# Performance work log

Hardware: AMD Instinct MI355X
Metric: run time of the kernel (lower is better)

Reference implementation:

```python
import jax, jax.numpy as jnp
import numpy as np

V = 327696       # total nodes (4 graphs x 2 hemis x 40962 verts)
E = 1966080      # directed edges
C = 64           # feature dim
G = 4            # num graphs (subjects)
EPS = 1e-5


def setup_inputs() -> dict:
    key = jax.random.key(0)
    ks = jax.random.split(key, 10)
    x = jax.random.normal(ks[0], (V, C), dtype=jnp.float32)
    edge_index = jax.random.randint(ks[1], (2, E), 0, V, dtype=jnp.int64)
    batch = jnp.sort(jax.random.randint(ks[2], (V,), 0, G, dtype=jnp.int64))
    s = 1.0 / np.sqrt(C)
    return {
        "x": x,
        "edge_index": edge_index,
        "batch": batch,
        # GraphNorm 1 (PyG init: weight=1, bias=0, mean_scale=1)
        "norm1_w": jnp.ones((C,), jnp.float32),
        "norm1_b": jnp.zeros((C,), jnp.float32),
        "norm1_ms": jnp.ones((C,), jnp.float32),
        # SAGEConv linear layers: lin_l (on max-aggregated neighbors, with bias), lin_r (root, no bias)
        "lin_l_w": jax.random.uniform(ks[3], (C, C), jnp.float32, -s, s),
        "lin_l_b": jax.random.uniform(ks[4], (C,), jnp.float32, -s, s),
        "lin_r_w": jax.random.uniform(ks[5], (C, C), jnp.float32, -s, s),
        # GraphNorm 2
        "norm2_w": jnp.ones((C,), jnp.float32),
        "norm2_b": jnp.zeros((C,), jnp.float32),
        "norm2_ms": jnp.ones((C,), jnp.float32),
    }


def graph_norm(x, batch, weight, bias, mean_scale):
    # per-graph mean/var over nodes (PyG GraphNorm)
    ones = jnp.ones((x.shape[0], 1), x.dtype)
    cnt = jax.ops.segment_sum(ones, batch, num_segments=G)            # [G,1]
    mean = jax.ops.segment_sum(x, batch, num_segments=G) / cnt       # [G,C]
    centered = x - mean[batch] * mean_scale
    var = jax.ops.segment_sum(centered * centered, batch, num_segments=G) / cnt
    inv_std = jax.lax.rsqrt(var + EPS)
    return weight * centered * inv_std[batch] + bias


def sage_conv_max(x, edge_index, lin_l_w, lin_l_b, lin_r_w):
    src, dst = edge_index[0], edge_index[1]
    # scatter-max of source features onto destinations (irregular access)
    agg = jax.ops.segment_max(x[src], dst, num_segments=V)
    agg = jnp.where(jnp.isneginf(agg), 0.0, agg)  # nodes with no in-edges -> 0
    return agg @ lin_l_w + lin_l_b + x @ lin_r_w


def reference(x, edge_index, batch, norm1_w, norm1_b, norm1_ms,
              lin_l_w, lin_l_b, lin_r_w, norm2_w, norm2_b, norm2_ms):
    h = graph_norm(x, batch, norm1_w, norm1_b, norm1_ms)
    h = sage_conv_max(h, edge_index, lin_l_w, lin_l_b, lin_r_w)
    h = jax.nn.relu(x + h)
    h = graph_norm(h, batch, norm2_w, norm2_b, norm2_ms)
    return h
```

## Files before the change

### kernel.cpp

```cpp
#include <hip/hip_runtime.h>

#define V_NODES 327696
#define E_EDGES 1966080
#define C_DIM   64
#define G_NUM   4
#define EPS_GN  1e-5f
#define N_TILES (V_NODES/16)
#define SAGE_BLOCKS 2048
#define WAVES_TOTAL (SAGE_BLOCKS*4)
#define FILL_BLOCKS 512
#define H_BLOCKS 2048
#define NB_SCAN 1281
#define CH_SCAN2 6
#define PW 520
#define STAT_BLOCKS 2048
#define STAT_WAVES (STAT_BLOCKS*4)
#define TOTAL_F4 (V_NODES*16)
#define SW_CHUNK 640
#define HIST_BLOCKS 960
#define RED_BLOCKS 129
#define SROW 17
#define STAGE_PAD 1280

typedef short bf16x8 __attribute__((ext_vector_type(8)));
typedef float f32x4  __attribute__((ext_vector_type(4)));
typedef unsigned uintx4 __attribute__((ext_vector_type(4)));
typedef int intx4 __attribute__((ext_vector_type(4)));

__device__ __forceinline__ unsigned short f2bf(float f) {
    unsigned u = __float_as_uint(f);
    return (unsigned short)((u + 0x7FFFu + ((u >> 16) & 1u)) >> 16);
}
__device__ __forceinline__ unsigned short encbf(float f) {
    unsigned short b = f2bf(f);
    return b ^ (unsigned short)(0x8000u | ((b >> 15) * 0x7FFFu));
}
__device__ __forceinline__ unsigned decp(unsigned e) {
    unsigned s = e & 0x80008000u;
    unsigned m = (s >> 15) * 0x7FFFu;
    return e ^ ~m;
}

__global__ __launch_bounds__(256) void k_pre(const float* __restrict__ x,
                                             const int* __restrict__ batch,
                                             const int* __restrict__ ei,
                                             int* __restrict__ hist,
                                             unsigned short* __restrict__ rank,
                                             float* __restrict__ partial1) {
    __shared__ float red_s[256], red_q[256], red_c[G_NUM];
    if (blockIdx.x < HIST_BLOCKS) {
        const int t = blockIdx.x * 256 + threadIdx.x;
        const int* dst = ei + E_EDGES;
        const int e0 = t * 4;
        const int e1 = (E_EDGES / 2) + t * 4;
        intx4 a = *(const intx4*)(dst + e0);
        intx4 b = *(const intx4*)(dst + e1);
        int r0 = atomicAdd(&hist[a[0]], 1);
        int r1 = atomicAdd(&hist[a[1]], 1);
        int r2 = atomicAdd(&hist[a[2]], 1);
        int r3 = atomicAdd(&hist[a[3]], 1);
        int r4 = atomicAdd(&hist[b[0]], 1);
        int r5 = atomicAdd(&hist[b[1]], 1);
        int r6 = atomicAdd(&hist[b[2]], 1);
        int r7 = atomicAdd(&hist[b[3]], 1);
        ushort4 wa = { (unsigned short)r0, (unsigned short)r1,
                       (unsigned short)r2, (unsigned short)r3 };
        ushort4 wb = { (unsigned short)r4, (unsigned short)r5,
                       (unsigned short)r6, (unsigned short)r7 };
        *(ushort4*)(rank + e0) = wa;
        *(ushort4*)(rank + e1) = wb;
        return;
    }
    const int t = threadIdx.x;
    red_s[t] = 0.0f; red_q[t] = 0.0f;
    if (t < G_NUM) red_c[t] = 0.0f;
    __syncthreads();
    const int bid  = blockIdx.x - HIST_BLOCKS;
    const int w    = bid * 4 + (t >> 6);
    const int lane = t & 63;
    const int base = w * SW_CHUNK;
    const int end  = (w == STAT_WAVES - 1) ? TOTAL_F4 : base + SW_CHUNK;
    const int c4   = (lane & 15) << 2;
    const bool cntr = (lane & 15) == 0;
    const float4* x4p = (const float4*)x;
    const int g0 = batch[base >> 4];
    const int g1 = batch[(end - 1) >> 4];
    if (g0 == g1 && end == base + SW_CHUNK) {
        float4 su = {0,0,0,0}, qu = {0,0,0,0};
        #pragma unroll
        for (int it = 0; it < 10; it++) {
            float4 v = x4p[base + lane + it * 64];
            su.x += v.x; su.y += v.y; su.z += v.z; su.w += v.w;
            qu.x = fmaf(v.x, v.x, qu.x); qu.y = fmaf(v.y, v.y, qu.y);
            qu.z = fmaf(v.z, v.z, qu.z); qu.w = fmaf(v.w, v.w, qu.w);
        }
        int p = (g0 << 6) + c4;
        atomicAdd(&red_s[p],   su.x); atomicAdd(&red_q[p],   qu.x);
        atomicAdd(&red_s[p+1], su.y); atomicAdd(&red_q[p+1], qu.y);
        atomicAdd(&red_s[p+2], su.z); atomicAdd(&red_q[p+2], qu.z);
        atomicAdd(&red_s[p+3], su.w); atomicAdd(&red_q[p+3], qu.w);
        if (cntr) atomicAdd(&red_c[g0], 10.0f);
    } else {
        for (int idx = base + lane; idx < end; idx += 64) {
            float4 v = x4p[idx];
            int g = batch[idx >> 4];
            int p = (g << 6) + c4;
            atomicAdd(&red_s[p],   v.x); atomicAdd(&red_q[p],   v.x * v.x);
            atomicAdd(&red_s[p+1], v.y); atomicAdd(&red_q[p+1], v.y * v.y);
            atomicAdd(&red_s[p+2], v.z); atomicAdd(&red_q[p+2], v.z * v.z);
            atomicAdd(&red_s[p+3], v.w); atomicAdd(&red_q[p+3], v.w * v.w);
            if (cntr) atomicAdd(&red_c[g], 1.0f);
        }
    }
    __syncthreads();
    float* row = partial1 + (size_t)bid * PW;
    row[t] = red_s[t]; row[256 + t] = red_q[t];
    if (t < G_NUM) row[512 + t] = red_c[t];
}

__global__ __launch_bounds__(256) void k_rs1(const float* __restrict__ partial1,
                                             const int* __restrict__ hist,
                                             float* __restrict__ outs,
                                             float* __restrict__ outc,
                                             int* __restrict__ bsum) {
    if (blockIdx.x < RED_BLOCKS) {
        int e = blockIdx.x * 4 + (threadIdx.x >> 6);
        int lane = threadIdx.x & 63;
        if (e >= 516) return;
        float s = 0.0f;
        for (int b = lane; b < STAT_BLOCKS; b += 64) s += partial1[(size_t)b * PW + e];
        #pragma unroll
        for (int off = 1; off < 64; off <<= 1) s += __shfl_xor(s, off);
        if (lane == 0) { if (e < 512) outs[e] = s; else outc[e - 512] = s; }
        return;
    }
    __shared__ int s[256];
    int sb = blockIdx.x - RED_BLOCKS;
    int i = sb * 256 + threadIdx.x;
    s[threadIdx.x] = (i < V_NODES) ? hist[i] : 0;
    __syncthreads();
    for (int off = 128; off > 0; off >>= 1) {
        if (threadIdx.x < off) s[threadIdx.x] += s[threadIdx.x + off];
        __syncthreads();
    }
    if (threadIdx.x == 0) bsum[sb] = s[0];
}

__global__ __launch_bounds__(256) void k_params(const float* __restrict__ sum,
                                                const float* __restrict__ sumsq,
                                                const float* __restrict__ cnt,
                                                const float* __restrict__ w,
                                                const float* __restrict__ b,
                                                const float* __restrict__ ms,
                                                float* __restrict__ scale,
                                                float* __restrict__ shift,
                                                const float* __restrict__ Wl,
                                                const float* __restrict__ Wr,
                                                char* __restrict__ gWsw,
                                                int* __restrict__ bsum) {
    if (blockIdx.x == 0) {
        int t = threadIdx.x;
        int g = t >> 6, c = t & 63;
        float n    = cnt[g];
        float mean = sum[t] / n;
        float msq  = sumsq[t] / n;
        float m    = ms[c];
        float var  = msq - 2.0f*m*mean*mean + m*m*mean*mean;
        float inv  = rsqrtf(var + EPS_GN);
        float sc   = w[c] * inv;
        scale[t] = sc;
        shift[t] = b[c] - mean * m * sc;
        for (int i = threadIdx.x; i < C_DIM*C_DIM; i += 256) {
            int k = i >> 6, col = i & 63;
            int boff = (col*128 + k*2) ^ ((col & 7) << 4);
            *(unsigned short*)(gWsw + boff)        = f2bf(Wl[i]);
            *(unsigned short*)(gWsw + 8192 + boff) = f2bf(Wr[i]);
        }
    } else {
        __shared__ int s[256];
        int t = threadIdx.x;
        int loc[CH_SCAN2];
        int mysum = 0;
        #pragma unroll
        for (int j = 0; j < CH_SCAN2; j++) {
            int idx = t * CH_SCAN2 + j;
            loc[j] = (idx < NB_SCAN) ? bsum[idx] : 0;
            mysum += loc[j];
        }
        s[t] = mysum;
        __syncthreads();
        for (int off = 1; off < 256; off <<= 1) {
            int tmp = (t >= off) ? s[t - off] : 0;
            __syncthreads();
            s[t] += tmp;
            __syncthreads();
        }
        int ex = s[t] - mysum;
        #pragma unroll
        for (int j = 0; j < CH_SCAN2; j++) {
            int idx = t * CH_SCAN2 + j;
            if (idx < NB_SCAN) { bsum[idx] = ex; ex += loc[j]; }
        }
    }
}

__global__ __launch_bounds__(256) void k_scan3(const int* __restrict__ hist,
                                               const int* __restrict__ bsum,
                                               int* __restrict__ offs) {
    __shared__ int s[256];
    int t = threadIdx.x;
    int i = blockIdx.x * 256 + t;
    int v = (i < V_NODES) ? hist[i] : 0;
    s[t] = v;
    __syncthreads();
    for (int off = 1; off < 256; off <<= 1) {
        int tmp = (t >= off) ? s[t - off] : 0;
        __syncthreads();
        s[t] += tmp;
        __syncthreads();
    }
    int ex = s[t] - v + bsum[blockIdx.x];
    if (i < V_NODES) offs[i] = ex;
    if (i == 0) offs[V_NODES] = E_EDGES;
}

__global__ __launch_bounds__(256) void k_h_fill(const float* __restrict__ x,
                                                const int* __restrict__ batch,
                                                const float* __restrict__ scale1,
                                                const float* __restrict__ shift1,
                                                unsigned short* __restrict__ henc,
                                                const int* __restrict__ ei,
                                                const unsigned short* __restrict__ rank,
                                                const int* __restrict__ offs,
                                                int* __restrict__ slots) {
    if (blockIdx.x < FILL_BLOCKS) {
        int stride = FILL_BLOCKS * 256;
        for (int e = blockIdx.x * 256 + threadIdx.x; e < E_EDGES; e += stride) {
            int src = ei[e];
            int d   = ei[E_EDGES + e];
            slots[offs[d] + (int)rank[e]] = src | ((d & 15) << 27);
        }
        return;
    }
    __shared__ float sc[256], sh[256];
    sc[threadIdx.x] = scale1[threadIdx.x];
    sh[threadIdx.x] = shift1[threadIdx.x];
    __syncthreads();
    const int total = V_NODES * 16;
    int bid = blockIdx.x - FILL_BLOCKS;
    int stride = H_BLOCKS * 256;
    const float4* x4 = (const float4*)x;
    ushort4* h4 = (ushort4*)henc;
    for (int i = bid * 256 + threadIdx.x; i < total; i += stride) {
        int v  = i >> 4;
        int c4 = (i & 15) << 2;
        int g  = batch[v];
        int p  = (g << 6) | c4;
        float4 val = x4[i];
        ushort4 o;
        o.x = encbf(fmaf(val.x, sc[p],   sh[p]));
        o.y = encbf(fmaf(val.y, sc[p+1], sh[p+1]));
        o.z = encbf(fmaf(val.z, sc[p+2], sh[p+2]));
        o.w = encbf(fmaf(val.w, sc[p+3], sh[p+3]));
        h4[i] = o;
    }
}

__global__ __launch_bounds__(256) void k_sage(const unsigned short* __restrict__ henc,
                                              const float* __restrict__ x,
                                              const int* __restrict__ batch,
                                              const int* __restrict__ offs,
                                              const int* __restrict__ slots,
                                              const char* __restrict__ gWsw,
                                              const float* __restrict__ bl,
                                              float* __restrict__ out,
                                              float* __restrict__ partial2) {
    __shared__ char lds_w[16384];
    __shared__ float red_s[256], red_q[256];
    __shared__ unsigned stage[4][STAGE_PAD];
    {
        const float4* wsrc = (const float4*)gWsw;
        float4* wdst = (float4*)lds_w;
        for (int t = threadIdx.x; t < 1024; t += 256) wdst[t] = wsrc[t];
    }
    red_s[threadIdx.x] = 0.0f; red_q[threadIdx.x] = 0.0f;
    __syncthreads();

    const int lane = threadIdx.x & 63;
    const int wid  = threadIdx.x >> 6;
    const int lg = lane >> 4, lr = lane & 15;
    const int es = lane >> 3;
    const int ss = lane & 7;
    const char* hbase = (const char*)henc;
    unsigned* st_w = &stage[wid][0];

    float blv[4];
    #pragma unroll
    for (int cb = 0; cb < 4; cb++) blv[cb] = bl[cb*16 + lr];

    float su[4] = {0,0,0,0}, qu[4] = {0,0,0,0};
    int gc = -1;

    const int gwave = blockIdx.x * 4 + wid;
    for (int tile = gwave; tile < N_TILES; tile += WAVES_TOTAL) {
        const int rbase = tile << 4;
        #pragma unroll
        for (int z = 0; z < 5; z++)
            *(uintx4*)(st_w + z*256 + lane*4) = (uintx4){0,0,0,0};
        int o_lo = offs[rbase + lr];
        int o_hi = offs[rbase + lr + 1];
        bool has = o_hi > o_lo;
        int st_t = __shfl(o_lo, 0);
        int en_t = __shfl(o_hi, 15);
        __builtin_amdgcn_wave_barrier();
        for (int i = st_t; i < en_t; i += 8) {
            int ii = i + es;
            unsigned sv = (ii < en_t) ? (unsigned)slots[ii]
                                      : (0x80000000u | (unsigned)V_NODES);
            unsigned src = sv & 0x07FFFFFFu;
            unsigned row = sv >> 27;
            uintx4 hv = *(const uintx4*)(hbase + ((size_t)src << 7) + ss*16);
            unsigned cb0 = (ss << 3);
            #pragma unroll
            for (int j = 0; j < 4; j++) {
                atomicMax(&st_w[(cb0 + 2*j    ) * SROW + row], hv[j] & 0xFFFFu);
                atomicMax(&st_w[(cb0 + 2*j + 1) * SROW + row], hv[j] >> 16);
            }
        }
        __builtin_amdgcn_wave_barrier();
        unsigned e0[8], e1[8];
        #pragma unroll
        for (int jj = 0; jj < 8; jj++) {
            e0[jj] = st_w[(lg*8 + jj) * SROW + lr];
            e1[jj] = st_w[(32 + lg*8 + jj) * SROW + lr];
        }
        __builtin_amdgcn_wave_barrier();
        uintx4 d0, d1;
        d0[0] = e0[0] | (e0[1] << 16); d0[1] = e0[2] | (e0[3] << 16);
        d0[2] = e0[4] | (e0[5] << 16); d0[3] = e0[6] | (e0[7] << 16);
        d1[0] = e1[0] | (e1[1] << 16); d1[1] = e1[2] | (e1[3] << 16);
        d1[2] = e1[4] | (e1[5] << 16); d1[3] = e1[6] | (e1[7] << 16);
        const char* hr = hbase + ((size_t)(rbase + lr) << 7);
        uintx4 r0 = *(const uintx4*)(hr + lg*16);
        uintx4 r1 = *(const uintx4*)(hr + 64 + lg*16);
        #pragma unroll
        for (int j = 0; j < 4; j++) {
            d0[j] = has ? decp(d0[j]) : 0u;
            d1[j] = has ? decp(d1[j]) : 0u;
            r0[j] = decp(r0[j]);
            r1[j] = decp(r1[j]);
        }
        bf16x8 a_agg0 = __builtin_bit_cast(bf16x8, d0);
        bf16x8 a_agg1 = __builtin_bit_cast(bf16x8, d1);
        bf16x8 a_h0   = __builtin_bit_cast(bf16x8, r0);
        bf16x8 a_h1   = __builtin_bit_cast(bf16x8, r1);

        f32x4 acc[4];
        #pragma unroll
        for (int cb = 0; cb < 4; cb++) {
            acc[cb] = (f32x4){0.f,0.f,0.f,0.f};
            int wrow = cb*16 + lr;
            int sw   = (wrow & 7) << 4;
            int o0   = (wrow*128 +      lg*16) ^ sw;
            int o1   = (wrow*128 + 64 + lg*16) ^ sw;
            bf16x8 wl0 = *(const bf16x8*)(lds_w + o0);
            bf16x8 wl1 = *(const bf16x8*)(lds_w + o1);
            bf16x8 wr0 = *(const bf16x8*)(lds_w + 8192 + o0);
            bf16x8 wr1 = *(const bf16x8*)(lds_w + 8192 + o1);
            acc[cb] = __builtin_amdgcn_mfma_f32_16x16x32_bf16(a_agg0, wl0, acc[cb], 0,0,0);
            acc[cb] = __builtin_amdgcn_mfma_f32_16x16x32_bf16(a_agg1, wl1, acc[cb], 0,0,0);
            acc[cb] = __builtin_amdgcn_mfma_f32_16x16x32_bf16(a_h0,   wr0, acc[cb], 0,0,0);
            acc[cb] = __builtin_amdgcn_mfma_f32_16x16x32_bf16(a_h1,   wr1, acc[cb], 0,0,0);
        }

        int g0 = batch[rbase], g15 = batch[rbase + 15];
        if (g0 == g15) {
            if (g0 != gc) {
                if (gc >= 0) {
                    #pragma unroll
                    for (int cb = 0; cb < 4; cb++) {
                        atomicAdd(&red_s[(gc<<6) + cb*16 + lr], su[cb]);
                        atomicAdd(&red_q[(gc<<6) + cb*16 + lr], qu[cb]);
                        su[cb] = 0.0f; qu[cb] = 0.0f;
                    }
                }
                gc = g0;
            }
            #pragma unroll
            for (int r = 0; r < 4; r++) {
                int row = rbase + lg*4 + r;
                #pragma unroll
                for (int cb = 0; cb < 4; cb++) {
                    int col = cb*16 + lr;
                    float xv = x[(size_t)row * C_DIM + col];
                    float o  = fmaxf(xv + acc[cb][r] + blv[cb], 0.0f);
                    out[(size_t)row * C_DIM + col] = o;
                    su[cb] += o; qu[cb] = fmaf(o, o, qu[cb]);
                }
            }
        } else {
            #pragma unroll
            for (int r = 0; r < 4; r++) {
                int row = rbase + lg*4 + r;
                int g   = batch[row];
                #pragma unroll
                for (int cb = 0; cb < 4; cb++) {
                    int col = cb*16 + lr;
                    float xv = x[(size_t)row * C_DIM + col];
                    float o  = fmaxf(xv + acc[cb][r] + blv[cb], 0.0f);
                    out[(size_t)row * C_DIM + col] = o;
                    int p = (g << 6) | col;
                    atomicAdd(&red_s[p], o);
                    atomicAdd(&red_q[p], o * o);
                }
            }
        }
    }
    if (gc >= 0) {
        #pragma unroll
        for (int cb = 0; cb < 4; cb++) {
            atomicAdd(&red_s[(gc<<6) + cb*16 + lr], su[cb]);
            atomicAdd(&red_q[(gc<<6) + cb*16 + lr], qu[cb]);
        }
    }
    __syncthreads();
    float* row = partial2 + (size_t)blockIdx.x * PW;
    row[threadIdx.x]       = red_s[threadIdx.x];
    row[256 + threadIdx.x] = red_q[threadIdx.x];
}

__global__ __launch_bounds__(256) void k_red2p(const float* __restrict__ partial2,
                                               const float* __restrict__ cnt,
                                               const float* __restrict__ w,
                                               const float* __restrict__ b,
                                               const float* __restrict__ ms,
                                               float* __restrict__ scale2,
                                               float* __restrict__ shift2) {
    int e = blockIdx.x * 4 + (threadIdx.x >> 6);
    int lane = threadIdx.x & 63;
    float s = 0.0f, q = 0.0f;
    for (int bb = lane; bb < SAGE_BLOCKS; bb += 64) {
        s += partial2[(size_t)bb * PW + e];
        q += partial2[(size_t)bb * PW + 256 + e];
    }
    #pragma unroll
    for (int off = 1; off < 64; off <<= 1) {
        s += __shfl_xor(s, off);
        q += __shfl_xor(q, off);
    }
    if (lane == 0) {
        int g = e >> 6, c = e & 63;
        float n    = cnt[g];
        float mean = s / n;
        float msq  = q / n;
        float m    = ms[c];
        float var  = msq - 2.0f*m*mean*mean + m*m*mean*mean;
        float inv  = rsqrtf(var + EPS_GN);
        float sc   = w[c] * inv;
        scale2[e] = sc;
        shift2[e] = b[c] - mean * m * sc;
    }
}

__global__ __launch_bounds__(256) void k_final(float* __restrict__ out,
                                               const int* __restrict__ batch,
                                               const float* __restrict__ scale2,
                                               const float* __restrict__ shift2) {
    __shared__ float sc[256], sh[256];
    sc[threadIdx.x] = scale2[threadIdx.x];
    sh[threadIdx.x] = shift2[threadIdx.x];
    __syncthreads();
    const int total = V_NODES * 16;
    int stride = gridDim.x * 256;
    float4* o4 = (float4*)out;
    for (int i = blockIdx.x * 256 + threadIdx.x; i < total; i += stride) {
        int v  = i >> 4;
        int c4 = (i & 15) << 2;
        int g  = batch[v];
        int p  = (g << 6) | c4;
        float4 val = o4[i];
        val.x = fmaf(val.x, sc[p],   sh[p]);
        val.y = fmaf(val.y, sc[p+1], sh[p+1]);
        val.z = fmaf(val.z, sc[p+2], sh[p+2]);
        val.w = fmaf(val.w, sc[p+3], sh[p+3]);
        o4[i] = val;
    }
}

extern "C" void kernel_launch(void* const* d_in, const int* in_sizes, int n_in,
                              void* d_out, int out_size, void* d_ws, size_t ws_size,
                              hipStream_t stream) {
    const float* x     = (const float*)d_in[0];
    const int*   ei    = (const int*)  d_in[1];
    const int*   batch = (const int*)  d_in[2];
    const float* n1w   = (const float*)d_in[3];
    const float* n1b   = (const float*)d_in[4];
    const float* n1ms  = (const float*)d_in[5];
    const float* Wl    = (const float*)d_in[6];
    const float* blv   = (const float*)d_in[7];
    const float* Wr    = (const float*)d_in[8];
    const float* n2w   = (const float*)d_in[9];
    const float* n2b   = (const float*)d_in[10];
    const float* n2ms  = (const float*)d_in[11];
    float* out = (float*)d_out;

    char* w = (char*)d_ws;
    unsigned short* henc = (unsigned short*)w; w += (size_t)(V_NODES + 1) * C_DIM * 2;
    int* slots           = (int*)w;            w += (size_t)E_EDGES * 4 + 64;
    int* hist            = (int*)w;            w += (size_t)V_NODES * 4;
    int* offs            = (int*)w;            w += (size_t)(V_NODES + 1) * 4 + 12;
    unsigned short* rank = (unsigned short*)w; w += (size_t)E_EDGES * 2;
    int* bsum            = (int*)w;            w += 1536 * 4;
    char* gWsw           = w;                  w += 16384;
    float* partial1      = (float*)w;          w += (size_t)STAT_BLOCKS * PW * 4;
    float* partial2      = (float*)w;          w += (size_t)SAGE_BLOCKS * PW * 4;
    float* stats  = (float*)w;
    float* sum1   = stats;
    float* sumsq1 = stats + 256;
    float* cnt    = stats + 512;
    float* scale1 = stats + 576;
    float* shift1 = stats + 832;
    float* scale2 = stats + 1088;
    float* shift2 = stats + 1344;

    hipMemsetAsync(hist, 0, (size_t)V_NODES * sizeof(int), stream);
    hipMemsetAsync(henc + (size_t)V_NODES * C_DIM, 0, C_DIM * 2, stream);

    k_pre   <<<HIST_BLOCKS + STAT_BLOCKS, 256, 0, stream>>>(x, batch, ei, hist, rank, partial1);
    k_rs1   <<<RED_BLOCKS + NB_SCAN, 256, 0, stream>>>(partial1, hist, sum1, cnt, bsum);
    k_params<<<2,    256, 0, stream>>>(sum1, sumsq1, cnt, n1w, n1b, n1ms,
                                       scale1, shift1, Wl, Wr, gWsw, bsum);
    k_scan3 <<<NB_SCAN, 256, 0, stream>>>(hist, bsum, offs);
    k_h_fill<<<FILL_BLOCKS + H_BLOCKS, 256, 0, stream>>>(x, batch, scale1, shift1,
                                       henc, ei, rank, offs, slots);
    k_sage  <<<SAGE_BLOCKS, 256, 0, stream>>>(henc, x, batch, offs, slots,
                                       gWsw, blv, out, partial2);
    k_red2p <<<64,   256, 0, stream>>>(partial2, cnt, n2w, n2b, n2ms, scale2, shift2);
    k_final <<<2048, 256, 0, stream>>>(out, batch, scale2, shift2);
}
```

Before: 363.5 us.

## Replace LDS atomic-max staging with per-row register packed max; stage output in bf16

The SAGE aggregation no longer scatters neighbor features into a shared-memory staging buffer with per-element atomicMax. Each lane now walks its own destination row's CSR slot range and keeps running maxima in registers, using packed 16-bit max on the order-preserving bf16 encoding. Slots no longer carry the row tag. Separately, the pre-norm output is written as bf16 into workspace when space allows, and the final norm pass reads it back, roughly halving that intermediate traffic. The cost is extra loads per lane for rows of uneven length, plus bf16 rounding of the intermediate output before the second GraphNorm.

```diff
diff --git a/kernel.cpp b/kernel.cpp
--- a/kernel.cpp
+++ b/kernel.cpp
@@ -19,17 +19,19 @@
 #define SW_CHUNK 640
 #define HIST_BLOCKS 960
 #define RED_BLOCKS 129
-#define SROW 17
-#define STAGE_PAD 1280
 
 typedef short bf16x8 __attribute__((ext_vector_type(8)));
 typedef float f32x4  __attribute__((ext_vector_type(4)));
 typedef unsigned uintx4 __attribute__((ext_vector_type(4)));
 typedef int intx4 __attribute__((ext_vector_type(4)));
+typedef unsigned short u16x2 __attribute__((ext_vector_type(2)));
 
 __device__ __forceinline__ unsigned short f2bf(float f) {
     unsigned u = __float_as_uint(f);
     return (unsigned short)((u + 0x7FFFu + ((u >> 16) & 1u)) >> 16);
+}
+__device__ __forceinline__ float bf2f(unsigned short b) {
+    return __uint_as_float(((unsigned)b) << 16);
 }
 __device__ __forceinline__ unsigned short encbf(float f) {
     unsigned short b = f2bf(f);
@@ -39,6 +41,12 @@
     unsigned s = e & 0x80008000u;
     unsigned m = (s >> 15) * 0x7FFFu;
     return e ^ ~m;
+}
+__device__ __forceinline__ unsigned pkmaxu(unsigned a, unsigned b) {
+    u16x2 xa = __builtin_bit_cast(u16x2, a);
+    u16x2 xb = __builtin_bit_cast(u16x2, b);
+    u16x2 r  = __builtin_elementwise_max(xa, xb);
+    return __builtin_bit_cast(unsigned, r);
 }
 
 __global__ __launch_bounds__(256) void k_pre(const float* __restrict__ x,
@@ -238,7 +246,7 @@
         for (int e = blockIdx.x * 256 + threadIdx.x; e < E_EDGES; e += stride) {
             int src = ei[e];
             int d   = ei[E_EDGES + e];
-            slots[offs[d] + (int)rank[e]] = src | ((d & 15) << 27);
+            slots[offs[d] + (int)rank[e]] = src;
         }
         return;
     }
@@ -274,10 +282,11 @@
                                               const char* __restrict__ gWsw,
                                               const float* __restrict__ bl,
                                               float* __restrict__ out,
+                                              unsigned short* __restrict__ outbf,
+                                              int bfout,
                                               float* __restrict__ partial2) {
     __shared__ char lds_w[16384];
     __shared__ float red_s[256], red_q[256];
-    __shared__ unsigned stage[4][STAGE_PAD];
     {
         const float4* wsrc = (const float4*)gWsw;
         float4* wdst = (float4*)lds_w;
@@ -289,10 +298,7 @@
     const int lane = threadIdx.x & 63;
     const int wid  = threadIdx.x >> 6;
     const int lg = lane >> 4, lr = lane & 15;
-    const int es = lane >> 3;
-    const int ss = lane & 7;
     const char* hbase = (const char*)henc;
-    unsigned* st_w = &stage[wid][0];
 
     float blv[4];
     #pragma unroll
@@ -304,49 +310,52 @@
     const int gwave = blockIdx.x * 4 + wid;
     for (int tile = gwave; tile < N_TILES; tile += WAVES_TOTAL) {
         const int rbase = tile << 4;
-        #pragma unroll
-        for (int z = 0; z < 5; z++)
-            *(uintx4*)(st_w + z*256 + lane*4) = (uintx4){0,0,0,0};
-        int o_lo = offs[rbase + lr];
-        int o_hi = offs[rbase + lr + 1];
-        bool has = o_hi > o_lo;
-        int st_t = __shfl(o_lo, 0);
-        int en_t = __shfl(o_hi, 15);
-        __builtin_amdgcn_wave_barrier();
-        for (int i = st_t; i < en_t; i += 8) {
-            int ii = i + es;
-            unsigned sv = (ii < en_t) ? (unsigned)slots[ii]
-                                      : (0x80000000u | (unsigned)V_NODES);
-            unsigned src = sv & 0x07FFFFFFu;
-            unsigned row = sv >> 27;
-            uintx4 hv = *(const uintx4*)(hbase + ((size_t)src << 7) + ss*16);
-            unsigned cb0 = (ss << 3);
-            #pragma unroll
-            for (int j = 0; j < 4; j++) {
-                atomicMax(&st_w[(cb0 + 2*j    ) * SROW + row], hv[j] & 0xFFFFu);
-                atomicMax(&st_w[(cb0 + 2*j + 1) * SROW + row], hv[j] >> 16);
-            }
-        }
-        __builtin_amdgcn_wave_barrier();
-        unsigned e0[8], e1[8];
-        #pragma unroll
-        for (int jj = 0; jj < 8; jj++) {
-            e0[jj] = st_w[(lg*8 + jj) * SROW + lr];
-            e1[jj] = st_w[(32 + lg*8 + jj) * SROW + lr];
-        }
-        __builtin_amdgcn_wave_barrier();
-        uintx4 d0, d1;
-        d0[0] = e0[0] | (e0[1] << 16); d0[1] = e0[2] | (e0[3] << 16);
-        d0[2] = e0[4] | (e0[5] << 16); d0[3] = e0[6] | (e0[7] << 16);
-        d1[0] = e1[0] | (e1[1] << 16); d1[1] = e1[2] | (e1[3] << 16);
-        d1[2] = e1[4] | (e1[5] << 16); d1[3] = e1[6] | (e1[7] << 16);
-        const char* hr = hbase + ((size_t)(rbase + lr) << 7);
+        const int myrow = rbase + lr;
+        int st = offs[myrow];
+        int en = offs[myrow + 1];
+
+        const char* hr = hbase + ((unsigned)myrow << 7);
         uintx4 r0 = *(const uintx4*)(hr + lg*16);
         uintx4 r1 = *(const uintx4*)(hr + 64 + lg*16);
+
+        uintx4 mA0 = {0,0,0,0}, mA1 = {0,0,0,0};
+        uintx4 mB0 = {0,0,0,0}, mB1 = {0,0,0,0};
+        for (int i = st & ~7; __ballot(i < en) != 0ull; i += 8) {
+            intx4 qa = *(const intx4*)(slots + i);
+            intx4 qb = *(const intx4*)(slots + i + 4);
+            uintx4 a0[4], a1[4], b0[4], b1[4];
+            #pragma unroll
+            for (int e = 0; e < 4; e++) {
+                int ia = i + e;
+                unsigned idxa = (ia >= st && ia < en) ? (unsigned)qa[e] : (unsigned)V_NODES;
+                const char* pa = hbase + ((size_t)idxa << 7);
+                a0[e] = *(const uintx4*)(pa + lg*16);
+                a1[e] = *(const uintx4*)(pa + 64 + lg*16);
+                int ib = i + 4 + e;
+                unsigned idxb = (ib >= st && ib < en) ? (unsigned)qb[e] : (unsigned)V_NODES;
+                const char* pb = hbase + ((size_t)idxb << 7);
+                b0[e] = *(const uintx4*)(pb + lg*16);
+                b1[e] = *(const uintx4*)(pb + 64 + lg*16);
+            }
+            #pragma unroll
+            for (int e = 0; e < 4; e++) {
+                #pragma unroll
+                for (int j = 0; j < 4; j++) {
+                    mA0[j] = pkmaxu(mA0[j], a0[e][j]);
+                    mA1[j] = pkmaxu(mA1[j], a1[e][j]);
+                    mB0[j] = pkmaxu(mB0[j], b0[e][j]);
+                    mB1[j] = pkmaxu(mB1[j], b1[e][j]);
+                }
+            }
+        }
+        bool has = en > st;
+        uintx4 d0, d1;
         #pragma unroll
         for (int j = 0; j < 4; j++) {
-            d0[j] = has ? decp(d0[j]) : 0u;
-            d1[j] = has ? decp(d1[j]) : 0u;
+            unsigned m0 = pkmaxu(mA0[j], mB0[j]);
+            unsigned m1 = pkmaxu(mA1[j], mB1[j]);
+            d0[j] = has ? decp(m0) : 0u;
+            d1[j] = has ? decp(m1) : 0u;
             r0[j] = decp(r0[j]);
             r1[j] = decp(r1[j]);
         }
@@ -394,7 +403,8 @@
                     int col = cb*16 + lr;
                     float xv = x[(size_t)row * C_DIM + col];
                     float o  = fmaxf(xv + acc[cb][r] + blv[cb], 0.0f);
-                    out[(size_t)row * C_DIM + col] = o;
+                    if (bfout) outbf[(size_t)row * C_DIM + col] = f2bf(o);
+                    else       out[(size_t)row * C_DIM + col] = o;
                     su[cb] += o; qu[cb] = fmaf(o, o, qu[cb]);
                 }
             }
@@ -408,7 +418,8 @@
                     int col = cb*16 + lr;
                     float xv = x[(size_t)row * C_DIM + col];
                     float o  = fmaxf(xv + acc[cb][r] + blv[cb], 0.0f);
-                    out[(size_t)row * C_DIM + col] = o;
+                    if (bfout) outbf[(size_t)row * C_DIM + col] = f2bf(o);
+                    else       out[(size_t)row * C_DIM + col] = o;
                     int p = (g << 6) | col;
                     atomicAdd(&red_s[p], o);
                     atomicAdd(&red_q[p], o * o);
@@ -463,6 +474,8 @@
 }
 
 __global__ __launch_bounds__(256) void k_final(float* __restrict__ out,
+                                               const unsigned short* __restrict__ outbf,
+                                               int bfin,
                                                const int* __restrict__ batch,
                                                const float* __restrict__ scale2,
                                                const float* __restrict__ shift2) {
@@ -473,17 +486,34 @@
     const int total = V_NODES * 16;
     int stride = gridDim.x * 256;
     float4* o4 = (float4*)out;
-    for (int i = blockIdx.x * 256 + threadIdx.x; i < total; i += stride) {
-        int v  = i >> 4;
-        int c4 = (i & 15) << 2;
-        int g  = batch[v];
-        int p  = (g << 6) | c4;
-        float4 val = o4[i];
-        val.x = fmaf(val.x, sc[p],   sh[p]);
-        val.y = fmaf(val.y, sc[p+1], sh[p+1]);
-        val.z = fmaf(val.z, sc[p+2], sh[p+2]);
-        val.w = fmaf(val.w, sc[p+3], sh[p+3]);
-        o4[i] = val;
+    if (bfin) {
+        const ushort4* ob4 = (const ushort4*)outbf;
+        for (int i = blockIdx.x * 256 + threadIdx.x; i < total; i += stride) {
+            int v  = i >> 4;
+            int c4 = (i & 15) << 2;
+            int g  = batch[v];
+            int p  = (g << 6) | c4;
+            ushort4 u = ob4[i];
+            float4 res;
+            res.x = fmaf(bf2f(u.x), sc[p],   sh[p]);
+            res.y = fmaf(bf2f(u.y), sc[p+1], sh[p+1]);
+            res.z = fmaf(bf2f(u.z), sc[p+2], sh[p+2]);
+            res.w = fmaf(bf2f(u.w), sc[p+3], sh[p+3]);
+            o4[i] = res;
+        }
+    } else {
+        for (int i = blockIdx.x * 256 + threadIdx.x; i < total; i += stride) {
+            int v  = i >> 4;
+            int c4 = (i & 15) << 2;
+            int g  = batch[v];
+            int p  = (g << 6) | c4;
+            float4 val = o4[i];
+            val.x = fmaf(val.x, sc[p],   sh[p]);
+            val.y = fmaf(val.y, sc[p+1], sh[p+1]);
+            val.z = fmaf(val.z, sc[p+2], sh[p+2]);
+            val.w = fmaf(val.w, sc[p+3], sh[p+3]);
+            o4[i] = val;
+        }
     }
 }
 
@@ -514,7 +544,7 @@
     char* gWsw           = w;                  w += 16384;
     float* partial1      = (float*)w;          w += (size_t)STAT_BLOCKS * PW * 4;
     float* partial2      = (float*)w;          w += (size_t)SAGE_BLOCKS * PW * 4;
-    float* stats  = (float*)w;
+    float* stats  = (float*)w;                 w += 2048 * 4;
     float* sum1   = stats;
     float* sumsq1 = stats + 256;
     float* cnt    = stats + 512;
@@ -522,6 +552,9 @@
     float* shift1 = stats + 832;
     float* scale2 = stats + 1088;
     float* shift2 = stats + 1344;
+    unsigned short* outbf = (unsigned short*)w;
+    size_t need_bf = (size_t)(w - (char*)d_ws) + (size_t)V_NODES * C_DIM * 2;
+    int bfout = (ws_size >= need_bf) ? 1 : 0;
 
     hipMemsetAsync(hist, 0, (size_t)V_NODES * sizeof(int), stream);
     hipMemsetAsync(henc + (size_t)V_NODES * C_DIM, 0, C_DIM * 2, stream);
@@ -534,7 +567,7 @@
     k_h_fill<<<FILL_BLOCKS + H_BLOCKS, 256, 0, stream>>>(x, batch, scale1, shift1,
                                        henc, ei, rank, offs, slots);
     k_sage  <<<SAGE_BLOCKS, 256, 0, stream>>>(henc, x, batch, offs, slots,
-                                       gWsw, blv, out, partial2);
+                                       gWsw, blv, out, outbf, bfout, partial2);
     k_red2p <<<64,   256, 0, stream>>>(partial2, cnt, n2w, n2b, n2ms, scale2, shift2);
-    k_final <<<2048, 256, 0, stream>>>(out, batch, scale2, shift2);
-}
+    k_final <<<2048, 256, 0, stream>>>(out, outbf, bfout, batch, scale2, shift2);
+}
```

Result: slower. 386.6 us (+6.4%).
